# Kernel optimization log

Measured on AMD Instinct MI355X. Metric: run time of the kernel, lower is better.

Reference implementation:

```python
import jax, jax.numpy as jnp
import numpy as np

EMB_DIM = 128
HEAD_SIZE = 16  # embDim // numHea = 128 // 8


def setup_inputs() -> dict:
    key = jax.random.key(0)
    k1, k2, k3, k4 = jax.random.split(key, 4)
    B, T = 8, 2048
    inpEmb = jax.random.normal(k1, (B, T, EMB_DIM), dtype=jnp.float32)
    # nn.Linear(embDim, heaSiz, bias=False) weights, stored transposed so y = x @ W
    Wq = jax.random.normal(k2, (EMB_DIM, HEAD_SIZE), dtype=jnp.float32) / np.sqrt(EMB_DIM)
    Wk = jax.random.normal(k3, (EMB_DIM, HEAD_SIZE), dtype=jnp.float32) / np.sqrt(EMB_DIM)
    Wv = jax.random.normal(k4, (EMB_DIM, HEAD_SIZE), dtype=jnp.float32) / np.sqrt(EMB_DIM)
    return {"inpEmb": inpEmb, "Wq": Wq, "Wk": Wk, "Wv": Wv}


def reference(inpEmb, Wq, Wk, Wv):
    # q,k,v: [B, T, H]
    q = inpEmb @ Wq
    k = inpEmb @ Wk
    v = inpEmb @ Wv
    scale = HEAD_SIZE ** -0.5
    # scores: [B, T, T]
    scores = jnp.einsum('bqh,bkh->bqk', q, k) * scale
    T = inpEmb.shape[1]
    causal = jnp.tril(jnp.ones((T, T), dtype=bool))
    scores = jnp.where(causal, scores, -jnp.inf)
    weights = jax.nn.softmax(scores, axis=-1)
    # dropout treated as identity (eval mode) for deterministic reference
    return jnp.einsum('bqk,bkh->bqh', weights, v)
```

## Files before the change

### kernel.cpp

```cpp
#include <hip/hip_runtime.h>
#include <hip/hip_bf16.h>

#define T_SEQ 2048
#define EMB   128
#define H     16
#define BATCH 8
#define VSTR  2064
#define QSCALE 0.360673760222241f

#define EXP2F(x) __builtin_amdgcn_exp2f(x)

typedef short short8_t __attribute__((ext_vector_type(8)));
typedef float f32x4    __attribute__((ext_vector_type(4)));

__device__ __forceinline__ unsigned short f2bf(float f) {
    __hip_bfloat16 h = __float2bfloat16(f);
    return *reinterpret_cast<unsigned short*>(&h);
}

__global__ __launch_bounds__(256) void qkv_kernel(
    const float* __restrict__ x,
    const float* __restrict__ Wq,
    const float* __restrict__ Wk,
    const float* __restrict__ Wv,
    unsigned short* __restrict__ Qbf,
    unsigned short* __restrict__ Kbf,
    unsigned short* __restrict__ Vt)
{
    __shared__ unsigned short Wt[3][16][136];

    const int tid = threadIdx.x;
#pragma unroll
    for (int p = 0; p < 6; ++p) {
        const int idx4 = tid + p * 256;
        const int flat = idx4 * 4;
        const int mm   = flat >> 11;
        const int rem  = flat & 2047;
        const int d    = rem >> 4;
        const int c0   = rem & 15;
        const float* Wm = (mm == 0) ? Wq : (mm == 1) ? Wk : Wv;
        float4 w = *reinterpret_cast<const float4*>(Wm + rem);
        Wt[mm][c0    ][d] = f2bf(w.x);
        Wt[mm][c0 + 1][d] = f2bf(w.y);
        Wt[mm][c0 + 2][d] = f2bf(w.z);
        Wt[mm][c0 + 3][d] = f2bf(w.w);
    }
    __syncthreads();

    const int wv   = tid >> 6;
    const int lane = tid & 63;
    const int q    = lane >> 4;
    const int n    = lane & 15;
    const int row0 = blockIdx.x * 64 + wv * 16;
    const float* xr = x + (size_t)(row0 + n) * EMB;

    f32x4 aq = {0,0,0,0}, ak = {0,0,0,0}, av = {0,0,0,0};
#pragma unroll
    for (int t = 0; t < 4; ++t) {
        const int k0 = t * 32 + q * 8;
        float4 xa = *reinterpret_cast<const float4*>(xr + k0);
        float4 xb = *reinterpret_cast<const float4*>(xr + k0 + 4);
        union { unsigned short s[8]; short8_t v; } xf;
        xf.s[0]=f2bf(xa.x); xf.s[1]=f2bf(xa.y); xf.s[2]=f2bf(xa.z); xf.s[3]=f2bf(xa.w);
        xf.s[4]=f2bf(xb.x); xf.s[5]=f2bf(xb.y); xf.s[6]=f2bf(xb.z); xf.s[7]=f2bf(xb.w);
        short8_t wqf = *reinterpret_cast<const short8_t*>(&Wt[0][n][k0]);
        short8_t wkf = *reinterpret_cast<const short8_t*>(&Wt[1][n][k0]);
        short8_t wvf = *reinterpret_cast<const short8_t*>(&Wt[2][n][k0]);
        aq = __builtin_amdgcn_mfma_f32_16x16x32_bf16(xf.v, wqf, aq, 0, 0, 0);
        ak = __builtin_amdgcn_mfma_f32_16x16x32_bf16(xf.v, wkf, ak, 0, 0, 0);
        av = __builtin_amdgcn_mfma_f32_16x16x32_bf16(xf.v, wvf, av, 0, 0, 0);
    }

    const int grow = row0 + q * 4;
    const int b    = grow >> 11;
    const int ib0  = grow & 2047;
#pragma unroll
    for (int r = 0; r < 4; ++r) {
        Qbf[(size_t)(grow + r) * H + n] = f2bf(aq[r] * QSCALE);
        Kbf[(size_t)(grow + r) * H + n] = f2bf(ak[r]);
    }
    union { unsigned short s[4]; unsigned long long u; } vp;
    vp.s[0]=f2bf(av[0]); vp.s[1]=f2bf(av[1]); vp.s[2]=f2bf(av[2]); vp.s[3]=f2bf(av[3]);
    *reinterpret_cast<unsigned long long*>(
        Vt + ((size_t)b * H + n) * VSTR + ib0) = vp.u;
}

__global__ __launch_bounds__(256) void attn_fused(
    const unsigned short* __restrict__ Qbf,
    const unsigned short* __restrict__ Kbf,
    const unsigned short* __restrict__ Vt,
    float* __restrict__ out)
{
    __shared__ unsigned int Pbuf[4][16][68];
    __shared__ float CombA[4][16][20];
    __shared__ float CombM[4][16];
    __shared__ float CombL[4][16];

    const int qt = blockIdx.x;
    const int b  = blockIdx.y;
    const int i0 = qt << 4;
    const int nc = (qt >> 3) + 1;

    const int tid  = threadIdx.x;
    const int wv   = tid >> 6;
    const int lane = tid & 63;
    const int q    = lane >> 4;
    const int n    = lane & 15;
    const int irow = i0 + n;

    const unsigned short* Qp = Qbf + (size_t)b * T_SEQ * H;
    const unsigned short* Kp = Kbf + (size_t)b * T_SEQ * H;
    const unsigned short* vrow = Vt + (size_t)b * H * VSTR + (size_t)n * VSTR;

    short8_t qf = {0,0,0,0,0,0,0,0};
    if (q < 2)
        qf = *reinterpret_cast<const short8_t*>(Qp + (size_t)irow * H + q * 8);

    f32x4 acc = {0.f, 0.f, 0.f, 0.f};
    float m = -1e30f;
    float l = 0.f;

    for (int c = wv; c < nc; c += 4) {
        const int j0 = c << 7;

        f32x4 S[8];
#pragma unroll
        for (int s = 0; s < 8; ++s) {
            short8_t kf = {0,0,0,0,0,0,0,0};
            if (q < 2)
                kf = *reinterpret_cast<const short8_t*>(
                        Kp + (size_t)(j0 + s * 16 + n) * H + q * 8);
            f32x4 z = {0.f, 0.f, 0.f, 0.f};
            S[s] = __builtin_amdgcn_mfma_f32_16x16x32_bf16(kf, qf, z, 0, 0, 0);
        }
        short8_t vf[4];
#pragma unroll
        for (int h = 0; h < 4; ++h)
            vf[h] = *reinterpret_cast<const short8_t*>(vrow + j0 + h * 32 + q * 8);

        float tm = -1e30f;
        if (j0 + 127 > i0) {
#pragma unroll
            for (int s = 0; s < 8; ++s) {
                const int kb = j0 + s * 16 + q * 4;
#pragma unroll
                for (int rr = 0; rr < 4; ++rr) {
                    float v = (kb + rr <= irow) ? S[s][rr] : -1e30f;
                    S[s][rr] = v;
                    tm = fmaxf(tm, v);
                }
            }
        } else {
#pragma unroll
            for (int s = 0; s < 8; ++s)
                tm = fmaxf(tm, fmaxf(fmaxf(S[s][0], S[s][1]),
                                     fmaxf(S[s][2], S[s][3])));
        }
        tm = fmaxf(tm, __shfl_xor(tm, 16));
        tm = fmaxf(tm, __shfl_xor(tm, 32));

        const float mn = fmaxf(m, tm);
        const float rs = EXP2F(m - mn);
        m = mn;
        acc[0] *= rs; acc[1] *= rs; acc[2] *= rs; acc[3] *= rs;

        float lc = 0.f;
#pragma unroll
        for (int s = 0; s < 8; ++s) {
            float e0 = EXP2F(S[s][0] - mn);
            float e1 = EXP2F(S[s][1] - mn);
            float e2 = EXP2F(S[s][2] - mn);
            float e3 = EXP2F(S[s][3] - mn);
            lc += (e0 + e1) + (e2 + e3);
            unsigned int b0 = __builtin_bit_cast(unsigned int, e0);
            unsigned int b1 = __builtin_bit_cast(unsigned int, e1);
            unsigned int b2 = __builtin_bit_cast(unsigned int, e2);
            unsigned int b3 = __builtin_bit_cast(unsigned int, e3);
            unsigned long long pw =
                (unsigned long long)((b1 & 0xffff0000u) | (b0 >> 16)) |
                ((unsigned long long)((b3 & 0xffff0000u) | (b2 >> 16)) << 32);
            *reinterpret_cast<unsigned long long*>(&Pbuf[wv][n][8 * s + 2 * q]) = pw;
        }
        l = l * rs + lc;

#pragma unroll
        for (int h = 0; h < 4; ++h) {
            uint4 p4 = *reinterpret_cast<const uint4*>(&Pbuf[wv][n][16 * h + 4 * q]);
            union { uint4 u; short8_t v; } pu; pu.u = p4;
            acc = __builtin_amdgcn_mfma_f32_16x16x32_bf16(vf[h], pu.v, acc, 0, 0, 0);
        }
    }

    l += __shfl_xor(l, 16);
    l += __shfl_xor(l, 32);

    *reinterpret_cast<float4*>(&CombA[wv][n][4 * q]) =
        (float4){acc[0], acc[1], acc[2], acc[3]};
    if (q == 0) { CombM[wv][n] = m; CombL[wv][n] = l; }
    __syncthreads();

    {
        const int row = tid >> 4;
        const int d   = tid & 15;
        float M = -1e30f;
#pragma unroll
        for (int w = 0; w < 4; ++w) M = fmaxf(M, CombM[w][row]);
        float L = 0.f, O = 0.f;
#pragma unroll
        for (int w = 0; w < 4; ++w) {
            const float wgt = EXP2F(CombM[w][row] - M);
            L += wgt * CombL[w][row];
            O += wgt * CombA[w][row][d];
        }
        out[((size_t)b * T_SEQ + i0 + row) * H + d] = O / L;
    }
}

extern "C" void kernel_launch(void* const* d_in, const int* in_sizes, int n_in,
                              void* d_out, int out_size, void* d_ws, size_t ws_size,
                              hipStream_t stream)
{
    const float* x  = (const float*)d_in[0];
    const float* Wq = (const float*)d_in[1];
    const float* Wk = (const float*)d_in[2];
    const float* Wv = (const float*)d_in[3];
    float* out = (float*)d_out;

    const size_t NE = (size_t)BATCH * T_SEQ * H;
    unsigned short* Qbf = (unsigned short*)d_ws;
    unsigned short* Kbf = Qbf + NE;
    unsigned short* Vt  = Kbf + NE;

    qkv_kernel<<<BATCH * T_SEQ / 64, 256, 0, stream>>>(
        x, Wq, Wk, Wv, Qbf, Kbf, Vt);
    attn_fused<<<dim3(T_SEQ / 16, BATCH), 256, 0, stream>>>(Qbf, Kbf, Vt, out);
}
```

Before: 81.63 us.

## Prefetch next K chunk in attention loop and restructure QKV projection per-wave

The attention loop now loads the K fragments for the next chunk into registers while the current chunk is processed, so global load latency overlaps with the softmax and PV work. The QKV kernel drops the shared-memory weight staging. Each of its three waves now computes one of Q, K or V for 16 rows, reading weights straight from global memory with strided scalar loads. attn_fused also gains an occupancy hint via launch_bounds(256,4). In exchange, the prefetch raises register pressure, the QKV kernel now loads x three times per row group, and its weight reads are uncoalesced.

```diff
diff --git a/kernel.cpp b/kernel.cpp
--- a/kernel.cpp
+++ b/kernel.cpp
@@ -18,7 +18,7 @@
     return *reinterpret_cast<unsigned short*>(&h);
 }
 
-__global__ __launch_bounds__(256) void qkv_kernel(
+__global__ __launch_bounds__(192) void qkv_kernel(
     const float* __restrict__ x,
     const float* __restrict__ Wq,
     const float* __restrict__ Wk,
@@ -27,34 +27,17 @@
     unsigned short* __restrict__ Kbf,
     unsigned short* __restrict__ Vt)
 {
-    __shared__ unsigned short Wt[3][16][136];
-
-    const int tid = threadIdx.x;
-#pragma unroll
-    for (int p = 0; p < 6; ++p) {
-        const int idx4 = tid + p * 256;
-        const int flat = idx4 * 4;
-        const int mm   = flat >> 11;
-        const int rem  = flat & 2047;
-        const int d    = rem >> 4;
-        const int c0   = rem & 15;
-        const float* Wm = (mm == 0) ? Wq : (mm == 1) ? Wk : Wv;
-        float4 w = *reinterpret_cast<const float4*>(Wm + rem);
-        Wt[mm][c0    ][d] = f2bf(w.x);
-        Wt[mm][c0 + 1][d] = f2bf(w.y);
-        Wt[mm][c0 + 2][d] = f2bf(w.z);
-        Wt[mm][c0 + 3][d] = f2bf(w.w);
-    }
-    __syncthreads();
-
+    const int tid  = threadIdx.x;
     const int wv   = tid >> 6;
     const int lane = tid & 63;
     const int q    = lane >> 4;
     const int n    = lane & 15;
-    const int row0 = blockIdx.x * 64 + wv * 16;
-    const float* xr = x + (size_t)(row0 + n) * EMB;
-
-    f32x4 aq = {0,0,0,0}, ak = {0,0,0,0}, av = {0,0,0,0};
+    const int r0   = blockIdx.x * 16;
+
+    const float* Wm = (wv == 0) ? Wq : (wv == 1) ? Wk : Wv;
+    const float* xr = x + (size_t)(r0 + n) * EMB;
+
+    f32x4 a = {0.f, 0.f, 0.f, 0.f};
 #pragma unroll
     for (int t = 0; t < 4; ++t) {
         const int k0 = t * 32 + q * 8;
@@ -63,29 +46,33 @@
         union { unsigned short s[8]; short8_t v; } xf;
         xf.s[0]=f2bf(xa.x); xf.s[1]=f2bf(xa.y); xf.s[2]=f2bf(xa.z); xf.s[3]=f2bf(xa.w);
         xf.s[4]=f2bf(xb.x); xf.s[5]=f2bf(xb.y); xf.s[6]=f2bf(xb.z); xf.s[7]=f2bf(xb.w);
-        short8_t wqf = *reinterpret_cast<const short8_t*>(&Wt[0][n][k0]);
-        short8_t wkf = *reinterpret_cast<const short8_t*>(&Wt[1][n][k0]);
-        short8_t wvf = *reinterpret_cast<const short8_t*>(&Wt[2][n][k0]);
-        aq = __builtin_amdgcn_mfma_f32_16x16x32_bf16(xf.v, wqf, aq, 0, 0, 0);
-        ak = __builtin_amdgcn_mfma_f32_16x16x32_bf16(xf.v, wkf, ak, 0, 0, 0);
-        av = __builtin_amdgcn_mfma_f32_16x16x32_bf16(xf.v, wvf, av, 0, 0, 0);
-    }
-
-    const int grow = row0 + q * 4;
-    const int b    = grow >> 11;
-    const int ib0  = grow & 2047;
-#pragma unroll
-    for (int r = 0; r < 4; ++r) {
-        Qbf[(size_t)(grow + r) * H + n] = f2bf(aq[r] * QSCALE);
-        Kbf[(size_t)(grow + r) * H + n] = f2bf(ak[r]);
-    }
-    union { unsigned short s[4]; unsigned long long u; } vp;
-    vp.s[0]=f2bf(av[0]); vp.s[1]=f2bf(av[1]); vp.s[2]=f2bf(av[2]); vp.s[3]=f2bf(av[3]);
-    *reinterpret_cast<unsigned long long*>(
-        Vt + ((size_t)b * H + n) * VSTR + ib0) = vp.u;
-}
-
-__global__ __launch_bounds__(256) void attn_fused(
+        union { unsigned short s[8]; short8_t v; } wf;
+#pragma unroll
+        for (int j = 0; j < 8; ++j)
+            wf.s[j] = f2bf(Wm[(size_t)(k0 + j) * H + n]);
+        a = __builtin_amdgcn_mfma_f32_16x16x32_bf16(xf.v, wf.v, a, 0, 0, 0);
+    }
+
+    const int grow = r0 + q * 4;
+    if (wv == 0) {
+#pragma unroll
+        for (int r = 0; r < 4; ++r)
+            Qbf[(size_t)(grow + r) * H + n] = f2bf(a[r] * QSCALE);
+    } else if (wv == 1) {
+#pragma unroll
+        for (int r = 0; r < 4; ++r)
+            Kbf[(size_t)(grow + r) * H + n] = f2bf(a[r]);
+    } else {
+        const int b   = grow >> 11;
+        const int ib0 = grow & 2047;
+        union { unsigned short s[4]; unsigned long long u; } vp;
+        vp.s[0]=f2bf(a[0]); vp.s[1]=f2bf(a[1]); vp.s[2]=f2bf(a[2]); vp.s[3]=f2bf(a[3]);
+        *reinterpret_cast<unsigned long long*>(
+            Vt + ((size_t)b * H + n) * VSTR + ib0) = vp.u;
+    }
+}
+
+__global__ __launch_bounds__(256, 4) void attn_fused(
     const unsigned short* __restrict__ Qbf,
     const unsigned short* __restrict__ Kbf,
     const unsigned short* __restrict__ Vt,
@@ -120,18 +107,34 @@
     float m = -1e30f;
     float l = 0.f;
 
-    for (int c = wv; c < nc; c += 4) {
+    int c = wv;
+    short8_t kcur[8];
+#pragma unroll
+    for (int s = 0; s < 8; ++s) kcur[s] = (short8_t){0,0,0,0,0,0,0,0};
+    if (c < (int)nc && q < 2) {
         const int j0 = c << 7;
+#pragma unroll
+        for (int s = 0; s < 8; ++s)
+            kcur[s] = *reinterpret_cast<const short8_t*>(
+                          Kp + (size_t)(j0 + s * 16 + n) * H + q * 8);
+    }
+
+    for (; c < nc; c += 4) {
+        const int j0 = c << 7;
 
         f32x4 S[8];
 #pragma unroll
         for (int s = 0; s < 8; ++s) {
-            short8_t kf = {0,0,0,0,0,0,0,0};
-            if (q < 2)
-                kf = *reinterpret_cast<const short8_t*>(
-                        Kp + (size_t)(j0 + s * 16 + n) * H + q * 8);
             f32x4 z = {0.f, 0.f, 0.f, 0.f};
-            S[s] = __builtin_amdgcn_mfma_f32_16x16x32_bf16(kf, qf, z, 0, 0, 0);
+            S[s] = __builtin_amdgcn_mfma_f32_16x16x32_bf16(kcur[s], qf, z, 0, 0, 0);
+        }
+        const int c2 = c + 4;
+        if (c2 < nc && q < 2) {
+            const int j2 = c2 << 7;
+#pragma unroll
+            for (int s = 0; s < 8; ++s)
+                kcur[s] = *reinterpret_cast<const short8_t*>(
+                              Kp + (size_t)(j2 + s * 16 + n) * H + q * 8);
         }
         short8_t vf[4];
 #pragma unroll
@@ -231,7 +234,7 @@
     unsigned short* Kbf = Qbf + NE;
     unsigned short* Vt  = Kbf + NE;
 
-    qkv_kernel<<<BATCH * T_SEQ / 64, 256, 0, stream>>>(
+    qkv_kernel<<<BATCH * T_SEQ / 16, 192, 0, stream>>>(
         x, Wq, Wk, Wv, Qbf, Kbf, Vt);
     attn_fused<<<dim3(T_SEQ / 16, BATCH), 256, 0, stream>>>(Qbf, Kbf, Vt, out);
 }
```

Measured after the change: 76.82 us. -5.9%, faster.
